# Performance work log

Hardware: AMD Instinct MI355X
Metric: run time of the kernel (lower is better)

Reference implementation:

```python
import jax, jax.numpy as jnp
import numpy as np

BLOCK_SIZE = 64

def quantize_dequantize(w, block_size=BLOCK_SIZE):
    # LPBQ double quantization: block-wise abs-max -> uint4 scale1 over fp32 scale2
    out_ch, in_ch = w.shape
    pad_len = (block_size - in_ch % block_size) % block_size
    if pad_len > 0:
        w = jnp.pad(w, ((0, 0), (0, pad_len)))
    wr = w.reshape(out_ch, -1, block_size)                      # [O, nB, B]
    s1 = jnp.clip(jnp.max(jnp.abs(wr), axis=-1, keepdims=True) / 7.0, 1e-8)   # [O, nB, 1]
    s2 = jnp.clip(jnp.max(s1, axis=1, keepdims=True) / 15.0, 1e-8)            # [O, 1, 1]
    s1_q = jnp.clip(jnp.round(s1 / s2), 0.0, 15.0)
    s1_recon = s1_q * s2
    w_q = jnp.clip(jnp.round(wr / s1_recon), -8.0, 7.0)
    w_recon = (w_q * s1_recon).reshape(out_ch, -1)
    if pad_len > 0:
        w_recon = w_recon[:, :-pad_len]
    return w_recon

def setup_inputs() -> dict:
    key = jax.random.key(0)
    k1, k2, k3 = jax.random.split(key, 3)
    B, S, IN, OUT = 1, 128, 4096, 11008
    x = jax.random.normal(k1, (B, S, IN), dtype=jnp.float32)
    weight = jax.random.normal(k2, (OUT, IN), dtype=jnp.float32)
    bias = jax.random.normal(k3, (OUT,), dtype=jnp.float32)
    return {"x": x, "weight": weight, "bias": bias}

def reference(x, weight, bias):
    w_q = quantize_dequantize(weight)
    # F.linear: x @ w_q.T + bias
    return jnp.einsum('bsi,oi->bso', x, w_q) + bias
```

## Files before the change

### kernel.cpp

```cpp
#include <hip/hip_runtime.h>
#include <hip/hip_bf16.h>

#define IN_CH 4096
#define OUT_CH 11008
#define QBLK 64

#define BM 128
#define BN 64
#define BK 64
#define KCHUNKS (IN_CH / BK)
#define KSPLIT 4
#define SPLIT_CHUNKS (KCHUNKS / KSPLIT)
#define NTILES (OUT_CH / BN)
#define XCONV_BLOCKS 16
#define BPAD 72

typedef short bf16x8 __attribute__((ext_vector_type(8)));
typedef float f32x4 __attribute__((ext_vector_type(4)));
typedef char char16v __attribute__((ext_vector_type(16)));

#define GLOBAL_AS __attribute__((address_space(1)))
#define LDS_AS __attribute__((address_space(3)))

__device__ inline unsigned short f2bf(float f) {
    union { __hip_bfloat16 h; unsigned short u; } cv;
    cv.h = __float2bfloat16(f);
    return cv.u;
}

__global__ __launch_bounds__(256) void quant_kernel(
        const float* __restrict__ w, const float* __restrict__ x,
        signed char* __restrict__ wq, float* __restrict__ s1rT,
        unsigned short* __restrict__ xq) {
    const int tid = threadIdx.x;

    if (blockIdx.x >= OUT_CH) {
        const int bx = blockIdx.x - OUT_CH;
        const float4* x4 = (const float4*)x;
        for (int it = 0; it < 32; ++it) {
            const int g = bx * 8192 + it * 256 + tid;
            float4 v = x4[g];
            ushort4 o;
            o.x = f2bf(v.x); o.y = f2bf(v.y); o.z = f2bf(v.z); o.w = f2bf(v.w);
            ((ushort4*)xq)[g] = o;
        }
        return;
    }

    const int row = blockIdx.x;
    const float* wrow = w + (size_t)row * IN_CH;
    signed char* orow = wq + (size_t)row * IN_CH;

    __shared__ float s1_lds[64];
    __shared__ float s2_lds;

    float4 v[4];
    const int lane16 = tid & 15;

    for (int p = 0; p < 4; ++p) {
        v[p] = ((const float4*)wrow)[p * 256 + tid];
        float m = fmaxf(fmaxf(fabsf(v[p].x), fabsf(v[p].y)),
                        fmaxf(fabsf(v[p].z), fabsf(v[p].w)));
        m = fmaxf(m, __shfl_xor(m, 1));
        m = fmaxf(m, __shfl_xor(m, 2));
        m = fmaxf(m, __shfl_xor(m, 4));
        m = fmaxf(m, __shfl_xor(m, 8));
        if (lane16 == 0)
            s1_lds[p * 16 + (tid >> 4)] = fmaxf(m * (1.0f / 7.0f), 1e-8f);
    }
    __syncthreads();

    if (tid < 64) {
        float s1 = s1_lds[tid];
        float m = s1;
        m = fmaxf(m, __shfl_xor(m, 1));
        m = fmaxf(m, __shfl_xor(m, 2));
        m = fmaxf(m, __shfl_xor(m, 4));
        m = fmaxf(m, __shfl_xor(m, 8));
        m = fmaxf(m, __shfl_xor(m, 16));
        m = fmaxf(m, __shfl_xor(m, 32));
        const float s2 = fmaxf(m * (1.0f / 15.0f), 1e-8f);
        const float s1q = fminf(fmaxf(rintf(s1 / s2), 0.0f), 15.0f);
        const float s1r = s1q * s2;
        s1_lds[tid] = s1r;
        s1rT[(size_t)tid * OUT_CH + row] = s1r;
    }
    __syncthreads();

    for (int p = 0; p < 4; ++p) {
        const float s1r = s1_lds[p * 16 + (tid >> 4)];
        char4 o;
        o.x = (signed char)(int)fminf(fmaxf(rintf(v[p].x / s1r), -8.0f), 7.0f);
        o.y = (signed char)(int)fminf(fmaxf(rintf(v[p].y / s1r), -8.0f), 7.0f);
        o.z = (signed char)(int)fminf(fmaxf(rintf(v[p].z / s1r), -8.0f), 7.0f);
        o.w = (signed char)(int)fminf(fmaxf(rintf(v[p].w / s1r), -8.0f), 7.0f);
        ((char4*)orow)[p * 256 + tid] = o;
    }
}

__global__ __launch_bounds__(256) void gemm_kernel(
        const unsigned short* __restrict__ A, const signed char* __restrict__ WQ,
        const float* __restrict__ s1rT, float* __restrict__ part) {
    __shared__ __align__(16) unsigned short ldsA[BM * BK];
    __shared__ __align__(16) unsigned short ldsB[BN * BPAD];

    const int tid = threadIdx.x;
    const int w = tid >> 6;
    const int l = tid & 63;
    const int wm = w >> 1;
    const int wn = w & 1;
    const int n0 = blockIdx.x * BN;
    const int kc0 = blockIdx.y * SPLIT_CHUNKS;

    const int r8 = l >> 3;
    const int sg = l & 7;

    const int brow = tid >> 2;
    const int bcg = tid & 3;

    f32x4 acc[4][2] = {};

    const int lane15 = l & 15;
    const int quad = l >> 4;

    for (int kc = kc0; kc < kc0 + SPLIT_CHUNKS; ++kc) {
        const int k0 = kc * BK;

        for (int i = 0; i < 4; ++i) {
            const unsigned short* gp =
                A + (size_t)(i * 32 + w * 8 + r8) * IN_CH + k0 + sg * 8;
            LDS_AS unsigned short* lp =
                (LDS_AS unsigned short*)&ldsA[(i * 32 + w * 8) * BK];
            __builtin_amdgcn_global_load_lds((const GLOBAL_AS void*)gp,
                                             (LDS_AS void*)lp, 16, 0, 0);
        }

        const float s1 = s1rT[(size_t)kc * OUT_CH + n0 + brow];
        char16v bq = *(const char16v*)(WQ + (size_t)(n0 + brow) * IN_CH +
                                       k0 + bcg * 16);
        bf16x8 o0, o1;
        for (int i = 0; i < 8; ++i)
            o0[i] = (short)f2bf((float)bq[i] * s1);
        for (int i = 0; i < 8; ++i)
            o1[i] = (short)f2bf((float)bq[8 + i] * s1);
        *(bf16x8*)&ldsB[brow * BPAD + bcg * 16] = o0;
        *(bf16x8*)&ldsB[brow * BPAD + bcg * 16 + 8] = o1;

        asm volatile("s_waitcnt vmcnt(0)" ::: "memory");
        __syncthreads();

        for (int kk = 0; kk < 2; ++kk) {
            bf16x8 af[4], bfv[2];
            const int ko = kk * 32 + quad * 8;
            for (int i = 0; i < 4; ++i)
                af[i] = *(const bf16x8*)&ldsA[(wm * 64 + i * 16 + lane15) * BK + ko];
            for (int j = 0; j < 2; ++j)
                bfv[j] = *(const bf16x8*)&ldsB[(wn * 32 + j * 16 + lane15) * BPAD + ko];
            for (int i = 0; i < 4; ++i)
                for (int j = 0; j < 2; ++j)
                    acc[i][j] = __builtin_amdgcn_mfma_f32_16x16x32_bf16(
                        af[i], bfv[j], acc[i][j], 0, 0, 0);
        }
        __syncthreads();
    }

    float* pbase = part + (size_t)blockIdx.y * BM * OUT_CH;
    const int m_base = wm * 64 + quad * 4;
    const int n_base = n0 + wn * 32 + lane15;
    for (int j = 0; j < 2; ++j) {
        for (int i = 0; i < 4; ++i) {
            const int m = m_base + i * 16;
            float* cp = pbase + (size_t)m * OUT_CH + n_base + j * 16;
            cp[0 * OUT_CH] = acc[i][j][0];
            cp[1 * OUT_CH] = acc[i][j][1];
            cp[2 * OUT_CH] = acc[i][j][2];
            cp[3 * OUT_CH] = acc[i][j][3];
        }
    }
}

__global__ __launch_bounds__(256) void reduce_kernel(
        const float* __restrict__ part, const float* __restrict__ bias,
        float* __restrict__ out) {
    const int m = blockIdx.y;
    const int x4 = blockIdx.x * 256 + threadIdx.x;
    if (x4 >= OUT_CH / 4) return;
    const size_t off = (size_t)m * OUT_CH + x4 * 4;

    float4 acc = ((const float4*)bias)[x4];
    for (int s = 0; s < KSPLIT; ++s) {
        float4 p = *(const float4*)(part + (size_t)s * BM * OUT_CH + off);
        acc.x += p.x; acc.y += p.y; acc.z += p.z; acc.w += p.w;
    }
    *(float4*)(out + off) = acc;
}

extern "C" void kernel_launch(void* const* d_in, const int* in_sizes, int n_in,
                              void* d_out, int out_size, void* d_ws, size_t ws_size,
                              hipStream_t stream) {
    const float* x = (const float*)d_in[0];
    const float* weight = (const float*)d_in[1];
    const float* bias = (const float*)d_in[2];
    float* out = (float*)d_out;

    signed char* wsQ = (signed char*)d_ws;
    unsigned short* wsX = (unsigned short*)(wsQ + (size_t)OUT_CH * IN_CH);
    float* wsS = (float*)(wsX + (size_t)BM * IN_CH);
    float* wsP = wsS + (size_t)QBLK * OUT_CH;

    quant_kernel<<<OUT_CH + XCONV_BLOCKS, 256, 0, stream>>>(weight, x, wsQ, wsS, wsX);
    gemm_kernel<<<dim3(NTILES, KSPLIT), 256, 0, stream>>>(wsX, wsQ, wsS, wsP);
    reduce_kernel<<<dim3((OUT_CH / 4 + 255) / 256, BM), 256, 0, stream>>>(
        wsP, bias, out);
}
```

Measured before the change: 297.7 us.

## Drop LDS staging in GEMM, load fragments directly to registers with double buffering

The GEMM no longer stages A and the dequantized B through shared memory with barriers. Each lane now loads its own MFMA fragments from global memory into registers, and two register-resident chunks are software-pipelined so the next chunk's loads overlap the current chunk's MFMAs. Weights are stored with a +8 offset as unsigned bytes so dequantization becomes a single FMA. The cost is redundant global and L2 traffic, since A rows are reloaded by both N-waves and B rows by both M-waves, and register pressure goes up.

Result: slower. 334.5 us (+12.4%).

```diff
diff --git a/kernel.cpp b/kernel.cpp
--- a/kernel.cpp
+++ b/kernel.cpp
@@ -13,14 +13,10 @@
 #define SPLIT_CHUNKS (KCHUNKS / KSPLIT)
 #define NTILES (OUT_CH / BN)
 #define XCONV_BLOCKS 16
-#define BPAD 72
 
 typedef short bf16x8 __attribute__((ext_vector_type(8)));
 typedef float f32x4 __attribute__((ext_vector_type(4)));
-typedef char char16v __attribute__((ext_vector_type(16)));
-
-#define GLOBAL_AS __attribute__((address_space(1)))
-#define LDS_AS __attribute__((address_space(3)))
+typedef unsigned int u32x2 __attribute__((ext_vector_type(2)));
 
 __device__ inline unsigned short f2bf(float f) {
     union { __hip_bfloat16 h; unsigned short u; } cv;
@@ -30,7 +26,7 @@
 
 __global__ __launch_bounds__(256) void quant_kernel(
         const float* __restrict__ w, const float* __restrict__ x,
-        signed char* __restrict__ wq, float* __restrict__ s1rT,
+        unsigned char* __restrict__ wq, float* __restrict__ s1rT,
         unsigned short* __restrict__ xq) {
     const int tid = threadIdx.x;
 
@@ -49,11 +45,9 @@
 
     const int row = blockIdx.x;
     const float* wrow = w + (size_t)row * IN_CH;
-    signed char* orow = wq + (size_t)row * IN_CH;
+    unsigned char* orow = wq + (size_t)row * IN_CH;
 
     __shared__ float s1_lds[64];
-    __shared__ float s2_lds;
-
     float4 v[4];
     const int lane16 = tid & 15;
 
@@ -89,85 +83,112 @@
 
     for (int p = 0; p < 4; ++p) {
         const float s1r = s1_lds[p * 16 + (tid >> 4)];
-        char4 o;
-        o.x = (signed char)(int)fminf(fmaxf(rintf(v[p].x / s1r), -8.0f), 7.0f);
-        o.y = (signed char)(int)fminf(fmaxf(rintf(v[p].y / s1r), -8.0f), 7.0f);
-        o.z = (signed char)(int)fminf(fmaxf(rintf(v[p].z / s1r), -8.0f), 7.0f);
-        o.w = (signed char)(int)fminf(fmaxf(rintf(v[p].w / s1r), -8.0f), 7.0f);
-        ((char4*)orow)[p * 256 + tid] = o;
-    }
+        uchar4 o;
+        o.x = (unsigned char)(int)(fminf(fmaxf(rintf(v[p].x / s1r), -8.0f), 7.0f) + 8.0f);
+        o.y = (unsigned char)(int)(fminf(fmaxf(rintf(v[p].y / s1r), -8.0f), 7.0f) + 8.0f);
+        o.z = (unsigned char)(int)(fminf(fmaxf(rintf(v[p].z / s1r), -8.0f), 7.0f) + 8.0f);
+        o.w = (unsigned char)(int)(fminf(fmaxf(rintf(v[p].w / s1r), -8.0f), 7.0f) + 8.0f);
+        ((uchar4*)orow)[p * 256 + tid] = o;
+    }
+}
+
+struct Chunk {
+    bf16x8 a[8];
+    u32x2 b[4];
+    float s[2];
+};
+
+__device__ inline void load_chunk(int kc, const unsigned short* __restrict__ Abase,
+                                  const unsigned char* __restrict__ Bbase,
+                                  const float* __restrict__ s1rT, int srow,
+                                  Chunk& c) {
+#pragma unroll
+    for (int i = 0; i < 4; ++i)
+#pragma unroll
+        for (int kk = 0; kk < 2; ++kk)
+            c.a[i * 2 + kk] =
+                *(const bf16x8*)(Abase + (size_t)i * 16 * IN_CH + kc * 64 + kk * 32);
+#pragma unroll
+    for (int j = 0; j < 2; ++j)
+#pragma unroll
+        for (int kk = 0; kk < 2; ++kk)
+            c.b[j * 2 + kk] =
+                *(const u32x2*)(Bbase + (size_t)j * 16 * IN_CH + kc * 64 + kk * 32);
+#pragma unroll
+    for (int j = 0; j < 2; ++j)
+        c.s[j] = s1rT[(size_t)kc * OUT_CH + srow + j * 16];
+}
+
+__device__ inline bf16x8 dq8(u32x2 u, float s1, float m8) {
+    bf16x8 r;
+#pragma unroll
+    for (int h = 0; h < 2; ++h) {
+        const unsigned int d = u[h];
+        r[h * 4 + 0] = (short)f2bf(__builtin_fmaf((float)((d >> 0) & 0xffu), s1, m8));
+        r[h * 4 + 1] = (short)f2bf(__builtin_fmaf((float)((d >> 8) & 0xffu), s1, m8));
+        r[h * 4 + 2] = (short)f2bf(__builtin_fmaf((float)((d >> 16) & 0xffu), s1, m8));
+        r[h * 4 + 3] = (short)f2bf(__builtin_fmaf((float)((d >> 24) & 0xffu), s1, m8));
+    }
+    return r;
+}
+
+__device__ inline void compute_chunk(const Chunk& c, f32x4 acc[4][2]) {
+    bf16x8 bq[4];
+#pragma unroll
+    for (int j = 0; j < 2; ++j) {
+        const float m8 = -8.0f * c.s[j];
+#pragma unroll
+        for (int kk = 0; kk < 2; ++kk)
+            bq[j * 2 + kk] = dq8(c.b[j * 2 + kk], c.s[j], m8);
+    }
+#pragma unroll
+    for (int kk = 0; kk < 2; ++kk)
+#pragma unroll
+        for (int i = 0; i < 4; ++i)
+#pragma unroll
+            for (int j = 0; j < 2; ++j)
+                acc[i][j] = __builtin_amdgcn_mfma_f32_16x16x32_bf16(
+                    c.a[i * 2 + kk], bq[j * 2 + kk], acc[i][j], 0, 0, 0);
 }
 
 __global__ __launch_bounds__(256) void gemm_kernel(
-        const unsigned short* __restrict__ A, const signed char* __restrict__ WQ,
+        const unsigned short* __restrict__ A, const unsigned char* __restrict__ WQ,
         const float* __restrict__ s1rT, float* __restrict__ part) {
-    __shared__ __align__(16) unsigned short ldsA[BM * BK];
-    __shared__ __align__(16) unsigned short ldsB[BN * BPAD];
-
     const int tid = threadIdx.x;
     const int w = tid >> 6;
     const int l = tid & 63;
     const int wm = w >> 1;
     const int wn = w & 1;
+    const int lane15 = l & 15;
+    const int quad = l >> 4;
     const int n0 = blockIdx.x * BN;
     const int kc0 = blockIdx.y * SPLIT_CHUNKS;
-
-    const int r8 = l >> 3;
-    const int sg = l & 7;
-
-    const int brow = tid >> 2;
-    const int bcg = tid & 3;
+    const int kcEnd = kc0 + SPLIT_CHUNKS;
+
+    const unsigned short* Abase = A + (size_t)(wm * 64 + lane15) * IN_CH + quad * 8;
+    const int srow = n0 + wn * 32 + lane15;
+    const unsigned char* Bbase = WQ + (size_t)srow * IN_CH + quad * 8;
 
     f32x4 acc[4][2] = {};
 
-    const int lane15 = l & 15;
-    const int quad = l >> 4;
-
-    for (int kc = kc0; kc < kc0 + SPLIT_CHUNKS; ++kc) {
-        const int k0 = kc * BK;
-
-        for (int i = 0; i < 4; ++i) {
-            const unsigned short* gp =
-                A + (size_t)(i * 32 + w * 8 + r8) * IN_CH + k0 + sg * 8;
-            LDS_AS unsigned short* lp =
-                (LDS_AS unsigned short*)&ldsA[(i * 32 + w * 8) * BK];
-            __builtin_amdgcn_global_load_lds((const GLOBAL_AS void*)gp,
-                                             (LDS_AS void*)lp, 16, 0, 0);
-        }
-
-        const float s1 = s1rT[(size_t)kc * OUT_CH + n0 + brow];
-        char16v bq = *(const char16v*)(WQ + (size_t)(n0 + brow) * IN_CH +
-                                       k0 + bcg * 16);
-        bf16x8 o0, o1;
-        for (int i = 0; i < 8; ++i)
-            o0[i] = (short)f2bf((float)bq[i] * s1);
-        for (int i = 0; i < 8; ++i)
-            o1[i] = (short)f2bf((float)bq[8 + i] * s1);
-        *(bf16x8*)&ldsB[brow * BPAD + bcg * 16] = o0;
-        *(bf16x8*)&ldsB[brow * BPAD + bcg * 16 + 8] = o1;
-
-        asm volatile("s_waitcnt vmcnt(0)" ::: "memory");
-        __syncthreads();
-
-        for (int kk = 0; kk < 2; ++kk) {
-            bf16x8 af[4], bfv[2];
-            const int ko = kk * 32 + quad * 8;
-            for (int i = 0; i < 4; ++i)
-                af[i] = *(const bf16x8*)&ldsA[(wm * 64 + i * 16 + lane15) * BK + ko];
-            for (int j = 0; j < 2; ++j)
-                bfv[j] = *(const bf16x8*)&ldsB[(wn * 32 + j * 16 + lane15) * BPAD + ko];
-            for (int i = 0; i < 4; ++i)
-                for (int j = 0; j < 2; ++j)
-                    acc[i][j] = __builtin_amdgcn_mfma_f32_16x16x32_bf16(
-                        af[i], bfv[j], acc[i][j], 0, 0, 0);
-        }
-        __syncthreads();
+    Chunk cur, nxt;
+    load_chunk(kc0, Abase, Bbase, s1rT, srow, cur);
+
+    for (int kc = kc0; kc < kcEnd; kc += 2) {
+        const int k1 = (kc + 1 < kcEnd) ? kc + 1 : kc;
+        const int k2 = (kc + 2 < kcEnd) ? kc + 2 : k1;
+        load_chunk(k1, Abase, Bbase, s1rT, srow, nxt);
+        compute_chunk(cur, acc);
+        load_chunk(k2, Abase, Bbase, s1rT, srow, cur);
+        compute_chunk(nxt, acc);
     }
 
     float* pbase = part + (size_t)blockIdx.y * BM * OUT_CH;
     const int m_base = wm * 64 + quad * 4;
     const int n_base = n0 + wn * 32 + lane15;
+#pragma unroll
     for (int j = 0; j < 2; ++j) {
+#pragma unroll
         for (int i = 0; i < 4; ++i) {
             const int m = m_base + i * 16;
             float* cp = pbase + (size_t)m * OUT_CH + n_base + j * 16;
@@ -203,7 +224,7 @@
     const float* bias = (const float*)d_in[2];
     float* out = (float*)d_out;
 
-    signed char* wsQ = (signed char*)d_ws;
+    unsigned char* wsQ = (unsigned char*)d_ws;
     unsigned short* wsX = (unsigned short*)(wsQ + (size_t)OUT_CH * IN_CH);
     float* wsS = (float*)(wsX + (size_t)BM * IN_CH);
     float* wsP = wsS + (size_t)QBLK * OUT_CH;
```
